# Kernel optimization log

Measured on AMD Instinct MI355X. Metric: run time of the kernel, lower is better.

## Reference

```python
import jax, jax.numpy as jnp
import numpy as np

SIGMA = 0.1  # kernel-point influence radius (KPConv linear correlation)


def setup_inputs() -> dict:
    key = jax.random.key(0)
    k1, k2, k3, k4, k5 = jax.random.split(key, 5)
    N, K, KP, CIN, COUT = 65536, 32, 15, 64, 128
    pos = jax.random.uniform(k1, (N, 3), dtype=jnp.float32)
    feats = jax.random.normal(k2, (N, CIN), dtype=jnp.float32)
    kernel_points = jax.random.normal(k3, (KP, 3), dtype=jnp.float32) * 0.05
    weights = jax.random.normal(k4, (KP, CIN, COUT), dtype=jnp.float32) / np.sqrt(KP * CIN)
    neighbors = jax.random.randint(k5, (N, K), 0, N, dtype=jnp.int64)
    return {"pos": pos, "feats": feats, "kernel_points": kernel_points,
            "weights": weights, "neighbors": neighbors}


def reference(pos, feats, kernel_points, weights, neighbors):
    # pos: [N,3], feats: [N,Cin], kernel_points: [Kp,3],
    # weights: [Kp,Cin,Cout], neighbors: [N,K] int
    neigh_pos = pos[neighbors]                      # [N,K,3] irregular gather
    rel = neigh_pos - pos[:, None, :]               # [N,K,3]
    # distance from each relative neighbor offset to each kernel point
    d = rel[:, :, None, :] - kernel_points[None, None, :, :]   # [N,K,Kp,3]
    dist = jnp.sqrt(jnp.sum(d * d, axis=-1))        # [N,K,Kp]
    infl = jnp.maximum(0.0, 1.0 - dist / SIGMA)     # linear correlation
    neigh_feat = feats[neighbors]                   # [N,K,Cin] irregular gather
    # per-kernel-point weighted neighbor aggregation, then projection
    weighted = jnp.einsum('njk,njc->nkc', infl, neigh_feat)    # [N,Kp,Cin]
    out = jnp.einsum('nkc,kcd->nd', weighted, weights)         # [N,Cout]
    return out
```

## Files before the change

kernel.cpp:

```cpp
#include <hip/hip_runtime.h>

#define NPTS  65536
#define KNB   32
#define KPn   15
#define CIN   64
#define COUT  128
#define MPTS  16
#define THREADS 512
#define WSTRIDE 968
#define NTILE 8
#define KSTEPS 30
#define WELEMS (NTILE * KSTEPS * 64 * 8)

typedef __attribute__((ext_vector_type(8))) short short8;
typedef __attribute__((ext_vector_type(4))) float f32x4;

__device__ __forceinline__ unsigned int f2bf(float f) {
    union { float f; unsigned int i; } v; v.f = f;
    return (v.i + 0x7fffu + ((v.i >> 16) & 1u)) >> 16;
}
__device__ __forceinline__ float rlanef(float v, int l) {
    union { float f; int i; } u; u.f = v;
    u.i = __builtin_amdgcn_readlane(u.i, l);
    return u.f;
}

__global__ void wtrans_kernel(const float* __restrict__ w,
                              const float* __restrict__ kpts,
                              unsigned short* __restrict__ wTf,
                              float4* __restrict__ kpq_out) {
    const int d = blockIdx.x * 256 + threadIdx.x;
    if (d < WELEMS) {
        const int j    = d & 7;
        const int lane = (d >> 3) & 63;
        const int ks   = (d >> 9) % KSTEPS;
        const int t    = d / (KSTEPS * 512);
        const int f    = ks * 32 + (lane >> 4) * 8 + j;
        const int cg   = f / 120;
        const int rem  = f - cg * 120;
        const int orig = (rem >> 3) * 64 + cg * 8 + (rem & 7);
        const int n    = t * 16 + (lane & 15);
        wTf[d] = (unsigned short)f2bf(w[(size_t)orig * COUT + n]);
    }
    if (blockIdx.x == 0 && threadIdx.x < 16) {
        const int k = threadIdx.x;
        if (k < KPn) {
            const float x = kpts[k * 3 + 0];
            const float y = kpts[k * 3 + 1];
            const float z = kpts[k * 3 + 2];
            kpq_out[k] = make_float4(x, y, z, x * x + y * y + z * z);
        } else {
            float mx = 0.f;
            for (int i = 0; i < KPn; ++i) {
                const float x = kpts[i * 3 + 0];
                const float y = kpts[i * 3 + 1];
                const float z = kpts[i * 3 + 2];
                mx = fmaxf(mx, x * x + y * y + z * z);
            }
            const float R = 0.1f + sqrtf(mx);
            kpq_out[15] = make_float4(R * R, 0.f, 0.f, 0.f);
        }
    }
}

#define PROC_HALF(MSK, ACC)                                                   \
    {                                                                         \
        unsigned long long msk_ = (MSK);                                      \
        while (msk_) {                                                        \
            const int j_ = (int)__builtin_ctzll(msk_);                        \
            msk_ &= msk_ - 1;                                                 \
            const int   nbs_ = __builtin_amdgcn_readlane(nbv, j_);            \
            const float rxs_ = rlanef(rx, j_);                                \
            const float rys_ = rlanef(ry, j_);                                \
            const float rzs_ = rlanef(rz, j_);                                \
            const float d2s_ = rlanef(d2r, j_);                               \
            const float f_   = feats[(size_t)nbs_ * CIN + lane];              \
            _Pragma("unroll")                                                 \
            for (int k = 0; k < KPn; ++k) {                                   \
                const float  dot = rxs_ * kpx[k] + rys_ * kpy[k] + rzs_ * kpz[k]; \
                if (dot > 0.5f * (d2s_ - 0.01f + kpw[k])) {                   \
                    const float dd = fmaxf(d2s_ - 2.f * dot + kpw[k], 0.f);   \
                    const float w_ = 1.0f - 10.0f * sqrtf(dd);                \
                    ACC[k] += w_ * f_;                                        \
                }                                                             \
            }                                                                 \
        }                                                                     \
    }

__global__ __launch_bounds__(THREADS, 8) void kpconv_kernel(
    const float* __restrict__ pos,
    const float* __restrict__ feats,
    const unsigned short* __restrict__ wTf,
    const float4* __restrict__ kpq_in,
    const int*   __restrict__ neighbors,
    float*       __restrict__ out)
{
    __shared__ __align__(16) unsigned short wl[MPTS * WSTRIDE];

    const int tid  = threadIdx.x;
    const int n0   = blockIdx.x * MPTS;
    const int lane = tid & 63;
    const int wv   = tid >> 6;
    const int m    = lane & 15;
    const int q    = lane >> 4;

    const int nbv = neighbors[(size_t)n0 * KNB + tid];
    const float px = pos[(size_t)nbv * 3 + 0];
    const float py = pos[(size_t)nbv * 3 + 1];
    const float pz = pos[(size_t)nbv * 3 + 2];

    float kpx[KPn], kpy[KPn], kpz[KPn], kpw[KPn];
    #pragma unroll
    for (int k = 0; k < KPn; ++k) {
        const float4 kp = kpq_in[k];
        kpx[k] = kp.x; kpy[k] = kp.y; kpz[k] = kp.z; kpw[k] = kp.w;
    }
    const float R2 = kpq_in[15].x;

    const int nAu = __builtin_amdgcn_readfirstlane(n0 + wv * 2);
    const float cxA = pos[(size_t)nAu * 3 + 0];
    const float cyA = pos[(size_t)nAu * 3 + 1];
    const float czA = pos[(size_t)nAu * 3 + 2];
    const float cxB = pos[(size_t)(nAu + 1) * 3 + 0];
    const float cyB = pos[(size_t)(nAu + 1) * 3 + 1];
    const float czB = pos[(size_t)(nAu + 1) * 3 + 2];

    const bool isA = (lane < 32);
    const float rx = px - (isA ? cxA : cxB);
    const float ry = py - (isA ? cyA : cyB);
    const float rz = pz - (isA ? czA : czB);
    const float d2r = rx * rx + ry * ry + rz * rz;

    const unsigned long long bal = __ballot(d2r < R2);

    float accA[KPn], accB[KPn];
    #pragma unroll
    for (int k = 0; k < KPn; ++k) { accA[k] = 0.f; accB[k] = 0.f; }

    PROC_HALF(bal & 0x00000000ffffffffull, accA);
    PROC_HALF(bal & 0xffffffff00000000ull, accB);

    {
        const int cg = lane >> 3, j = lane & 7;
        unsigned short* wpA = wl + (wv * 2 + 0) * WSTRIDE + cg * 120 + j;
        unsigned short* wpB = wl + (wv * 2 + 1) * WSTRIDE + cg * 120 + j;
        #pragma unroll
        for (int k = 0; k < KPn; ++k) {
            wpA[k * 8] = (unsigned short)f2bf(accA[k]);
            wpB[k * 8] = (unsigned short)f2bf(accB[k]);
        }
    }
    __syncthreads();

    {
        f32x4 o0 = {0.f, 0.f, 0.f, 0.f};
        f32x4 o1 = {0.f, 0.f, 0.f, 0.f};
        const unsigned short* ap = wl + m * WSTRIDE + q * 8;
        const short8* bp = (const short8*)wTf + (size_t)wv * KSTEPS * 64 + lane;

        #pragma unroll 3
        for (int ks = 0; ks < KSTEPS; ks += 2) {
            const short8 a0 = *(const short8*)(ap + ks * 32);
            const short8 b0 = bp[ks * 64];
            o0 = __builtin_amdgcn_mfma_f32_16x16x32_bf16(a0, b0, o0, 0, 0, 0);
            const short8 a1 = *(const short8*)(ap + (ks + 1) * 32);
            const short8 b1 = bp[(ks + 1) * 64];
            o1 = __builtin_amdgcn_mfma_f32_16x16x32_bf16(a1, b1, o1, 0, 0, 0);
        }
        o0 = o0 + o1;

        const int c = wv * 16 + m;
        #pragma unroll
        for (int r = 0; r < 4; ++r)
            out[(size_t)(n0 + q * 4 + r) * COUT + c] = o0[r];
    }
}

extern "C" void kernel_launch(void* const* d_in, const int* in_sizes, int n_in,
                              void* d_out, int out_size, void* d_ws, size_t ws_size,
                              hipStream_t stream) {
    const float* pos       = (const float*)d_in[0];
    const float* feats     = (const float*)d_in[1];
    const float* kpts      = (const float*)d_in[2];
    const float* weights   = (const float*)d_in[3];
    const int*   neighbors = (const int*)d_in[4];
    float*       out       = (float*)d_out;
    unsigned short* wTf    = (unsigned short*)d_ws;
    float4* kpq            = (float4*)((char*)d_ws + WELEMS * 2);

    wtrans_kernel<<<(WELEMS + 255) / 256, 256, 0, stream>>>(weights, kpts, wTf, kpq);
    kpconv_kernel<<<NPTS / MPTS, THREADS, 0, stream>>>(
        pos, feats, wTf, kpq, neighbors, out);
}
```

Baseline: 144.4 us.

## Compute kernel-point influences per lane and loop over per-kernel-point ballot masks

Each lane now computes the influence of its own neighbor on all 15 kernel points in parallel and packs them as 16-bit fixed-point values into registers. The old scheme broadcast each in-range neighbor's offset and evaluated all kernel points serially inside the wave. Accumulation now loops over kernel points and, for each one, only over the neighbors with nonzero influence, found by a ballot. This removes redundant scalarized geometry work and iterations that contribute zero. In exchange, the same feature row may be loaded several times (once per kernel point it touches), and the 16-bit quantization of the weights adds some precision loss.

Result: faster. 136.5 us (-5.5%).

```diff
diff --git a/kernel.cpp b/kernel.cpp
--- a/kernel.cpp
+++ b/kernel.cpp
@@ -18,11 +18,6 @@
 __device__ __forceinline__ unsigned int f2bf(float f) {
     union { float f; unsigned int i; } v; v.f = f;
     return (v.i + 0x7fffu + ((v.i >> 16) & 1u)) >> 16;
-}
-__device__ __forceinline__ float rlanef(float v, int l) {
-    union { float f; int i; } u; u.f = v;
-    u.i = __builtin_amdgcn_readlane(u.i, l);
-    return u.f;
 }
 
 __global__ void wtrans_kernel(const float* __restrict__ w,
@@ -63,27 +58,18 @@
     }
 }
 
-#define PROC_HALF(MSK, ACC)                                                   \
+#define ACC_HALF(MHALF, BASE, ACCV)                                           \
     {                                                                         \
-        unsigned long long msk_ = (MSK);                                      \
-        while (msk_) {                                                        \
-            const int j_ = (int)__builtin_ctzll(msk_);                        \
-            msk_ &= msk_ - 1;                                                 \
-            const int   nbs_ = __builtin_amdgcn_readlane(nbv, j_);            \
-            const float rxs_ = rlanef(rx, j_);                                \
-            const float rys_ = rlanef(ry, j_);                                \
-            const float rzs_ = rlanef(rz, j_);                                \
-            const float d2s_ = rlanef(d2r, j_);                               \
-            const float f_   = feats[(size_t)nbs_ * CIN + lane];              \
-            _Pragma("unroll")                                                 \
-            for (int k = 0; k < KPn; ++k) {                                   \
-                const float  dot = rxs_ * kpx[k] + rys_ * kpy[k] + rzs_ * kpz[k]; \
-                if (dot > 0.5f * (d2s_ - 0.01f + kpw[k])) {                   \
-                    const float dd = fmaxf(d2s_ - 2.f * dot + kpw[k], 0.f);   \
-                    const float w_ = 1.0f - 10.0f * sqrtf(dd);                \
-                    ACC[k] += w_ * f_;                                        \
-                }                                                             \
-            }                                                                 \
+        unsigned long long mh_ = (MHALF);                                     \
+        while (mh_) {                                                         \
+            const int j_ = (int)__builtin_ctzll(mh_) + (BASE);                \
+            mh_ &= mh_ - 1;                                                   \
+            const int nb_ = __builtin_amdgcn_readlane(nbv, j_);               \
+            const unsigned int wp_ =                                          \
+                (unsigned int)__builtin_amdgcn_readlane((int)wpk[k >> 1], j_);\
+            const float w_ = (float)((wp_ >> (16 * (k & 1))) & 0xFFFFu) *     \
+                             (1.0f / 65535.0f);                               \
+            ACCV += w_ * feats[(size_t)nb_ * CIN + lane];                     \
         }                                                                     \
     }
 
@@ -109,14 +95,6 @@
     const float py = pos[(size_t)nbv * 3 + 1];
     const float pz = pos[(size_t)nbv * 3 + 2];
 
-    float kpx[KPn], kpy[KPn], kpz[KPn], kpw[KPn];
-    #pragma unroll
-    for (int k = 0; k < KPn; ++k) {
-        const float4 kp = kpq_in[k];
-        kpx[k] = kp.x; kpy[k] = kp.y; kpz[k] = kp.z; kpw[k] = kp.w;
-    }
-    const float R2 = kpq_in[15].x;
-
     const int nAu = __builtin_amdgcn_readfirstlane(n0 + wv * 2);
     const float cxA = pos[(size_t)nAu * 3 + 0];
     const float cyA = pos[(size_t)nAu * 3 + 1];
@@ -131,23 +109,33 @@
     const float rz = pz - (isA ? czA : czB);
     const float d2r = rx * rx + ry * ry + rz * rz;
 
-    const unsigned long long bal = __ballot(d2r < R2);
-
-    float accA[KPn], accB[KPn];
+    unsigned int kmask = 0;
+    unsigned int wpk[8] = {0u, 0u, 0u, 0u, 0u, 0u, 0u, 0u};
     #pragma unroll
-    for (int k = 0; k < KPn; ++k) { accA[k] = 0.f; accB[k] = 0.f; }
-
-    PROC_HALF(bal & 0x00000000ffffffffull, accA);
-    PROC_HALF(bal & 0xffffffff00000000ull, accB);
+    for (int k = 0; k < KPn; ++k) {
+        const float4 kp  = kpq_in[k];
+        const float  dot = rx * kp.x + ry * kp.y + rz * kp.z;
+        if (dot > 0.5f * (d2r - 0.01f + kp.w)) {
+            const float dd = fmaxf(d2r - 2.f * dot + kp.w, 0.f);
+            const float w  = 1.0f - 10.0f * sqrtf(dd);
+            const unsigned int w16 = (unsigned int)(w * 65535.0f + 0.5f);
+            wpk[k >> 1] |= w16 << (16 * (k & 1));
+            kmask |= 1u << k;
+        }
+    }
 
     {
-        const int cg = lane >> 3, j = lane & 7;
-        unsigned short* wpA = wl + (wv * 2 + 0) * WSTRIDE + cg * 120 + j;
-        unsigned short* wpB = wl + (wv * 2 + 1) * WSTRIDE + cg * 120 + j;
+        const int cg = lane >> 3, j8 = lane & 7;
+        unsigned short* const wpA = wl + (wv * 2 + 0) * WSTRIDE + cg * 120 + j8;
+        unsigned short* const wpB = wl + (wv * 2 + 1) * WSTRIDE + cg * 120 + j8;
         #pragma unroll
         for (int k = 0; k < KPn; ++k) {
-            wpA[k * 8] = (unsigned short)f2bf(accA[k]);
-            wpB[k * 8] = (unsigned short)f2bf(accB[k]);
+            const unsigned long long mk = __ballot((kmask >> k) & 1u);
+            float aA = 0.f, aB = 0.f;
+            ACC_HALF(mk & 0x00000000ffffffffull, 0, aA);
+            ACC_HALF(mk >> 32, 32, aB);
+            wpA[k * 8] = (unsigned short)f2bf(aA);
+            wpB[k * 8] = (unsigned short)f2bf(aB);
         }
     }
     __syncthreads();
```
